# Performance work log

Measured on AMD Instinct MI355X. Metric: run time of the kernel, lower is better.

## Reference

```python
import jax, jax.numpy as jnp
import numpy as np

T_STEPS = 128
N_RAYS = 16384
RAY_EXT = 10.0  # ray_ext_factor


def _posenc(x, n_freq=4):
    # x: (...,3) in [-1,1] -> (...,3 + 3*2*n_freq) = (...,27)
    feats = [x]
    for k in range(n_freq):
        f = (2.0 ** k) * jnp.pi
        feats.append(jnp.sin(f * x))
        feats.append(jnp.cos(f * x))
    return jnp.concatenate(feats, -1)


def _sh_deg2(d):
    # real spherical harmonics, degree 0 and 1 (4 coeffs), d unit vectors (...,3)
    x, y, z = d[..., 0], d[..., 1], d[..., 2]
    c0 = 0.28209479177387814
    c1 = 0.4886025119029199
    return jnp.stack([jnp.full_like(x, c0), c1 * y, c1 * z, c1 * x], -1)


def _forward(rays_o, rays_d, tnoise, aabb, W1, b1, W2, b2, Wc1, bc1, Wc2, bc2):
    # --- ray-AABB intersection (slab method), RayBundle.intersect_aabb ---
    inv_d = 1.0 / rays_d
    t0 = (aabb[0] - rays_o) * inv_d
    t1 = (aabb[1] - rays_o) * inv_d
    tnear = jnp.maximum(jnp.max(jnp.minimum(t0, t1), -1, keepdims=True), 0.0)  # (N,1)
    tfar = jnp.min(jnp.maximum(t0, t1), -1, keepdims=True)                      # (N,1)
    active = (tfar > tnear).astype(rays_o.dtype)  # active_mask; masking replaces compaction

    # --- StratifiedRayStepSampler: ts (T,N,1) ---
    T = tnoise.shape[0]
    base = (jnp.arange(T, dtype=rays_o.dtype)[:, None, None] + tnoise) / T
    ts = tnear[None] + (tfar - tnear)[None] * base
    xyz = rays_o[None] + ts * rays_d[None]  # (T,N,3)

    # --- vol.sample(xyz, ynm, return_color=True): density + color MLP ---
    xn = 2.0 * (xyz - aabb[0]) / (aabb[1] - aabb[0]) - 1.0
    enc = _posenc(xn)                             # (T,N,27)
    h = jax.nn.relu(enc @ W1 + b1)                # (T,N,64)
    dh = h @ W2 + b2                              # (T,N,16)
    sigma = jnp.exp(dh[..., :1])                  # (T,N,1) density
    feat = dh[..., 1:]                            # (T,N,15)
    dnorm = jnp.linalg.norm(rays_d, axis=-1, keepdims=True)  # (N,1)
    ynm = _sh_deg2(rays_d / dnorm)                # encode_raydir -> (N,4)
    ynm = jnp.broadcast_to(ynm[None], (T,) + ynm.shape)      # expand to (T,N,4)
    hc = jax.nn.relu(jnp.concatenate([feat, ynm], -1) @ Wc1 + bc1)
    rgb = jax.nn.sigmoid(hc @ Wc2 + bc2)          # (T,N,3)

    # --- integrate_timesteps: transmittance-weighted compositing ---
    tfinal = tfar * RAY_EXT
    delta = jnp.concatenate([ts[1:] - ts[:-1], tfinal[None] - ts[-1:]], 0)  # (T,N,1)
    sd = sigma * delta * dnorm[None]
    alpha = 1.0 - jnp.exp(-sd)
    trans = jnp.exp(-(jnp.cumsum(sd, 0) - sd))    # exclusive cumsum transmittance
    w = trans * alpha * active[None]              # (T,N,1); inactive rays -> zero maps

    color = jnp.sum(w * rgb, 0)                   # color_map  (N,3)
    alpha_map = jnp.sum(w, 0)                     # alpha_map  (N,1)
    return jnp.concatenate([color, alpha_map], -1)  # rgba (N,4)


def setup_inputs() -> dict:
    key = jax.random.key(0)
    ks = jax.random.split(key, 8)
    # origins on a sphere of radius 2.5 around the unit aabb, aimed at points inside it
    o = jax.random.normal(ks[0], (N_RAYS, 3), jnp.float32)
    o = 2.5 * o / jnp.linalg.norm(o, axis=-1, keepdims=True)
    tgt = jax.random.uniform(ks[1], (N_RAYS, 3), jnp.float32, -0.5, 0.5)
    d = tgt - o
    d = d / jnp.linalg.norm(d, axis=-1, keepdims=True)
    aabb = jnp.array([[-1.0, -1.0, -1.0], [1.0, 1.0, 1.0]], jnp.float32)
    tnoise = jax.random.uniform(ks[2], (T_STEPS, N_RAYS, 1), jnp.float32)
    s1, s2, s3, s4 = 27 ** -0.5, 64 ** -0.5, 19 ** -0.5, 64 ** -0.5
    return {
        'rays_o': o, 'rays_d': d, 'tnoise': tnoise, 'aabb': aabb,
        'W1': jax.random.normal(ks[3], (27, 64), jnp.float32) * s1,
        'b1': jnp.zeros((64,), jnp.float32),
        'W2': jax.random.normal(ks[4], (64, 16), jnp.float32) * (0.1 * s2),
        'b2': jnp.zeros((16,), jnp.float32),
        'Wc1': jax.random.normal(ks[5], (19, 64), jnp.float32) * s3,
        'bc1': jnp.zeros((64,), jnp.float32),
        'Wc2': jax.random.normal(ks[6], (64, 3), jnp.float32) * s4,
        'bc2': jnp.zeros((3,), jnp.float32),
    }


def reference(rays_o, rays_d, tnoise, aabb, W1, b1, W2, b2, Wc1, bc1, Wc2, bc2):
    return _forward(rays_o, rays_d, tnoise, aabb, W1, b1, W2, b2, Wc1, bc1, Wc2, bc2)
```

## Files before the change

### kernel.cpp

```cpp
#include <hip/hip_runtime.h>
#include <stdint.h>

#define N_RAYS  16384
#define T_STEPS 128
#define RPW   16
#define WAVES 4
#define TSEG  32

typedef _Float16 half8  __attribute__((ext_vector_type(8)));
typedef _Float16 half4  __attribute__((ext_vector_type(4)));
typedef __fp16   fp16x2 __attribute__((ext_vector_type(2)));
typedef float    float4_ __attribute__((ext_vector_type(4)));
typedef uint32_t uint2_  __attribute__((ext_vector_type(2)));

#define H8_W1    0
#define H8_W2    256
#define H8_WC2   384
#define H_WC1K16 4096
#define F32_CV   3072
#define F32_BC2  3392
#define F32_S0   3408

__device__ __forceinline__ uint32_t pk(float a, float b) {
    fp16x2 h = __builtin_amdgcn_cvt_pkrtz(a, b);
    return __builtin_bit_cast(uint32_t, h);
}
__device__ __forceinline__ uint32_t pkr(float a, float b) {
    fp16x2 h = __builtin_amdgcn_cvt_pkrtz(a, b);
    fp16x2 z = {(__fp16)0.f, (__fp16)0.f};
    fp16x2 m = __builtin_elementwise_max(h, z);
    return __builtin_bit_cast(uint32_t, m);
}

__global__ void prep_weights(const float* __restrict__ W1, const float* __restrict__ b1,
                             const float* __restrict__ W2, const float* __restrict__ b2,
                             const float* __restrict__ Wc1, const float* __restrict__ bc1,
                             const float* __restrict__ Wc2, const float* __restrict__ bc2,
                             void* __restrict__ ws) {
    _Float16* wh = (_Float16*)ws;
    float*    wf = (float*)ws;
    int frag = blockIdx.x;
    int lane = threadIdx.x;
    int mm = lane & 15, q = lane >> 4;
    if (frag < 4) {
        int tau = frag;
        int n = tau * 16 + mm;
        for (int j = 0; j < 8; ++j) {
            float w;
            if (j < 6)      w = W1[(3 + 6 * q + j) * 64 + n];
            else if (j == 6) w = (q == 0) ? W1[0 * 64 + n] : (q == 1) ? W1[2 * 64 + n] : 0.f;
            else             w = (q == 0) ? W1[1 * 64 + n] : (q == 1) ? b1[n] : 0.f;
            wh[(H8_W1 + tau * 64 + lane) * 8 + j] = (_Float16)w;
        }
    } else if (frag < 6) {
        int kap = frag - 4;
        for (int j = 0; j < 8; ++j) {
            int k = kap * 32 + q * 8 + j;
            wh[(H8_W2 + kap * 64 + lane) * 8 + j] = (_Float16)W2[k * 16 + mm];
        }
    } else if (frag < 10) {
        int tau = frag - 6;
        int n2 = tau * 16 + mm;
        for (int j = 0; j < 4; ++j) {
            int k = 4 * q + j;
            float w = (k == 0) ? 0.f : Wc1[(k - 1) * 64 + n2];
            wh[H_WC1K16 + (tau * 64 + lane) * 4 + j] = (_Float16)w;
        }
    } else if (frag < 12) {
        int kap = frag - 10;
        for (int j = 0; j < 8; ++j) {
            int k = kap * 32 + q * 8 + j;
            wh[(H8_WC2 + kap * 64 + lane) * 8 + j] =
                (_Float16)((mm < 3) ? Wc2[k * 3 + mm] : 0.f);
        }
    } else {
        int n = lane;
        wf[F32_CV + 0 * 64 + n] = Wc1[15 * 64 + n];
        wf[F32_CV + 1 * 64 + n] = Wc1[16 * 64 + n];
        wf[F32_CV + 2 * 64 + n] = Wc1[17 * 64 + n];
        wf[F32_CV + 3 * 64 + n] = Wc1[18 * 64 + n];
        float cc = bc1[n];
        for (int c = 0; c < 15; ++c) cc += b2[1 + c] * Wc1[c * 64 + n];
        wf[F32_CV + 4 * 64 + n] = cc;
        if (lane < 16) wf[F32_BC2 + lane] = (lane < 3) ? bc2[lane] : 0.f;
        if (lane == 0) wf[F32_S0] = b2[0];
    }
}

__global__ __launch_bounds__(256, 4)
void render_kernel(const float* __restrict__ rays_o, const float* __restrict__ rays_d,
                   const float* __restrict__ tnoise, const float* __restrict__ aabb,
                   const void* __restrict__ ws, float* __restrict__ out) {
    __shared__ __align__(16) _Float16 sH[WAVES][2][1024];
    __shared__ float sComb[WAVES][RPW][5];

    const int tid  = threadIdx.x;
    const int wv   = tid >> 6;
    const int lane = tid & 63;
    const int m    = lane & 15;
    const int q    = lane >> 4;
    const int r    = blockIdx.x * RPW + m;

    const half8* wsv  = (const half8*)ws;
    const half4* wsv4 = (const half4*)((const _Float16*)ws + H_WC1K16);
    const float* wsf  = (const float*)ws;
    half8 fW1[4], fW2[2], fWc2[2];
    half4 fWc1[4];
    #pragma unroll
    for (int i = 0; i < 4; ++i) fW1[i]  = wsv[H8_W1  + i * 64 + lane];
    #pragma unroll
    for (int i = 0; i < 2; ++i) fW2[i]  = wsv[H8_W2  + i * 64 + lane];
    #pragma unroll
    for (int i = 0; i < 2; ++i) fWc2[i] = wsv[H8_WC2 + i * 64 + lane];
    #pragma unroll
    for (int i = 0; i < 4; ++i) fWc1[i] = wsv4[i * 64 + lane];
    const float4_ binit = ((const float4_*)(wsf + F32_BC2))[q];
    const float s0b = wsf[F32_S0];

    float o0 = rays_o[r * 3 + 0], o1 = rays_o[r * 3 + 1], o2 = rays_o[r * 3 + 2];
    float d0 = rays_d[r * 3 + 0], d1 = rays_d[r * 3 + 1], d2 = rays_d[r * 3 + 2];
    float a00 = aabb[0], a01 = aabb[1], a02 = aabb[2];
    float a10 = aabb[3], a11 = aabb[4], a12 = aabb[5];

    float i0 = 1.0f / d0, i1 = 1.0f / d1, i2 = 1.0f / d2;
    float u0 = (a00 - o0) * i0, v0 = (a10 - o0) * i0;
    float u1 = (a01 - o1) * i1, v1 = (a11 - o1) * i1;
    float u2 = (a02 - o2) * i2, v2 = (a12 - o2) * i2;
    float tnear = fmaxf(fmaxf(fmaxf(fminf(u0, v0), fminf(u1, v1)), fminf(u2, v2)), 0.0f);
    float tfar  = fminf(fminf(fmaxf(u0, v0), fmaxf(u1, v1)), fmaxf(u2, v2));
    bool active = (tfar > tnear);
    float dt = tfar - tnear;
    float dt128 = dt * (1.0f / 128.0f);

    float dn  = sqrtf(d0 * d0 + d1 * d1 + d2 * d2);
    float idn = 1.0f / dn;
    const float c0sh = 0.28209479177387814f;
    const float c1sh = 0.4886025119029199f;
    float y1 = c1sh * d1 * idn, y2 = c1sh * d2 * idn, y3 = c1sh * d0 * idn;

    float4_ cv[4];
    #pragma unroll
    for (int tau = 0; tau < 4; ++tau) {
        #pragma unroll
        for (int reg = 0; reg < 4; ++reg) {
            int n = tau * 16 + 4 * q + reg;
            float c = wsf[F32_CV + 4 * 64 + n];
            c = fmaf(c0sh, wsf[F32_CV + 0 * 64 + n], c);
            c = fmaf(y1,   wsf[F32_CV + 1 * 64 + n], c);
            c = fmaf(y2,   wsf[F32_CV + 2 * 64 + n], c);
            c = fmaf(y3,   wsf[F32_CV + 3 * 64 + n], c);
            cv[tau][reg] = c;
        }
    }

    float qs = 0.5f * (float)(1 << q);
    float sc0 = 2.0f / (a10 - a00), of0 = -a00 * sc0 - 1.0f;
    float sc1 = 2.0f / (a11 - a01), of1 = -a01 * sc1 - 1.0f;
    float sc2 = 2.0f / (a12 - a02), of2 = -a02 * sc2 - 1.0f;
    float scq0 = sc0 * qs, ofq0 = of0 * qs;
    float scq1 = sc1 * qs, ofq1 = of1 * qs;
    float scq2 = sc2 * qs, ofq2 = of2 * qs;

    _Float16*       hwp[2];
    const _Float16* hrp[2];
    #pragma unroll
    for (int p = 0; p < 2; ++p) {
        hwp[p] = &sH[wv][p][((q >> 1) * 16 + m) * 8 + 4 * (q & 1)];
        hrp[p] = &sH[wv][p][(q * 16 + m) * 8];
    }

    const float4_ z4 = {0.f, 0.f, 0.f, 0.f};
    const bool q0 = (q == 0), q1 = (q == 1);

    float trans = 1.0f, sdtot = 0.0f, wacc = 0.0f;
    float cacc0 = 0.0f, cacc1 = 0.0f, cacc2 = 0.0f;

    const int tbase = wv * TSEG;
    float nA = tnoise[(tbase + 0) * N_RAYS + r];
    float nB = tnoise[(tbase + 1) * N_RAYS + r];

    #pragma unroll 1
    for (int tt = 0; tt < TSEG; tt += 2) {
        const int t0 = tbase + tt, t1 = t0 + 1;
        float nC = (t0 + 2 < T_STEPS) ? tnoise[(t0 + 2) * N_RAYS + r] : 0.0f;
        float nD = (t0 + 3 < T_STEPS) ? tnoise[(t0 + 3) * N_RAYS + r] : 0.0f;
        float ts0 = fmaf((float)t0 + nA, dt128, tnear);
        float ts1 = fmaf((float)t1 + nB, dt128, tnear);
        float ts2 = fmaf((float)(t0 + 2) + nC, dt128, tnear);
        float tsP[2] = {ts0, ts1};
        float deltaP[2];
        deltaP[0] = ts1 - ts0;
        deltaP[1] = (t1 < T_STEPS - 1) ? (ts2 - ts1) : fmaf(tfar, 10.0f, -ts1);
        nA = nC; nB = nD;

        float dhx[2];
        float4_ rgbP[2];

        #pragma unroll
        for (int p = 0; p < 2; ++p) {
            float x = fmaf(tsP[p], d0, o0);
            float y = fmaf(tsP[p], d1, o1);
            float z = fmaf(tsP[p], d2, o2);
            float xr0 = fmaf(x, scq0, ofq0);
            float xr1 = fmaf(y, scq1, ofq1);
            float xr2 = fmaf(z, scq2, ofq2);
            float s0 = __builtin_amdgcn_sinf(xr0);
            float s1 = __builtin_amdgcn_sinf(xr1);
            float s2 = __builtin_amdgcn_sinf(xr2);
            float cA = __builtin_amdgcn_cosf(xr0);
            float cB = __builtin_amdgcn_cosf(xr1);
            float cC = __builtin_amdgcn_cosf(xr2);
            float e6 = q0 ? (xr0 + xr0) : (q1 ? xr2 : 0.0f);
            float e7 = q0 ? (xr1 + xr1) : (q1 ? 1.0f : 0.0f);
            union { uint32_t u[4]; half8 h; } xf_;
            xf_.u[0] = pk(s0, s1); xf_.u[1] = pk(s2, cA);
            xf_.u[2] = pk(cB, cC); xf_.u[3] = pk(e6, e7);
            half8 xf = xf_.h;

            float4_ h0 = __builtin_amdgcn_mfma_f32_16x16x32_f16(fW1[0], xf, z4, 0, 0, 0);
            float4_ h1 = __builtin_amdgcn_mfma_f32_16x16x32_f16(fW1[1], xf, z4, 0, 0, 0);
            float4_ h2 = __builtin_amdgcn_mfma_f32_16x16x32_f16(fW1[2], xf, z4, 0, 0, 0);
            float4_ h3 = __builtin_amdgcn_mfma_f32_16x16x32_f16(fW1[3], xf, z4, 0, 0, 0);
            uint2_ w;
            w.x = pkr(h0.x, h0.y); w.y = pkr(h0.z, h0.w); *(uint2_*)(hwp[p] + 0 * 256) = w;
            w.x = pkr(h1.x, h1.y); w.y = pkr(h1.z, h1.w); *(uint2_*)(hwp[p] + 1 * 256) = w;
            w.x = pkr(h2.x, h2.y); w.y = pkr(h2.z, h2.w); *(uint2_*)(hwp[p] + 2 * 256) = w;
            w.x = pkr(h3.x, h3.y); w.y = pkr(h3.z, h3.w); *(uint2_*)(hwp[p] + 3 * 256) = w;
        }

        #pragma unroll
        for (int p = 0; p < 2; ++p) {
            half8 hb0 = *(const half8*)(hrp[p] + 0);
            half8 hb1 = *(const half8*)(hrp[p] + 512);
            float4_ dh = __builtin_amdgcn_mfma_f32_16x16x32_f16(fW2[0], hb0, z4, 0, 0, 0);
            dh = __builtin_amdgcn_mfma_f32_16x16x32_f16(fW2[1], hb1, dh, 0, 0, 0);
            dhx[p] = dh.x;

            union { uint32_t u[2]; half4 h; } bf_;
            bf_.u[0] = pk(dh.x, dh.y); bf_.u[1] = pk(dh.z, dh.w);
            half4 fb = bf_.h;

            float4_ t0v = __builtin_amdgcn_mfma_f32_16x16x16f16(fWc1[0], fb, cv[0], 0, 0, 0);
            float4_ t1v = __builtin_amdgcn_mfma_f32_16x16x16f16(fWc1[1], fb, cv[1], 0, 0, 0);
            float4_ t2v = __builtin_amdgcn_mfma_f32_16x16x16f16(fWc1[2], fb, cv[2], 0, 0, 0);
            float4_ t3v = __builtin_amdgcn_mfma_f32_16x16x16f16(fWc1[3], fb, cv[3], 0, 0, 0);
            uint2_ w;
            w.x = pkr(t0v.x, t0v.y); w.y = pkr(t0v.z, t0v.w); *(uint2_*)(hwp[p] + 0 * 256) = w;
            w.x = pkr(t1v.x, t1v.y); w.y = pkr(t1v.z, t1v.w); *(uint2_*)(hwp[p] + 1 * 256) = w;
            w.x = pkr(t2v.x, t2v.y); w.y = pkr(t2v.z, t2v.w); *(uint2_*)(hwp[p] + 2 * 256) = w;
            w.x = pkr(t3v.x, t3v.y); w.y = pkr(t3v.z, t3v.w); *(uint2_*)(hwp[p] + 3 * 256) = w;
        }

        #pragma unroll
        for (int p = 0; p < 2; ++p) {
            half8 cb0 = *(const half8*)(hrp[p] + 0);
            half8 cb1 = *(const half8*)(hrp[p] + 512);
            float4_ rgbp = __builtin_amdgcn_mfma_f32_16x16x32_f16(fWc2[0], cb0, binit, 0, 0, 0);
            rgbP[p] = __builtin_amdgcn_mfma_f32_16x16x32_f16(fWc2[1], cb1, rgbp, 0, 0, 0);
        }

        if (q == 0) {
            #pragma unroll
            for (int p = 0; p < 2; ++p) {
                float sigma = __expf(dhx[p] + s0b);
                float sd = sigma * deltaP[p] * dn;
                float e = __expf(-sd);
                float alpha = 1.0f - e;
                float w = trans * alpha;
                float rr = __builtin_amdgcn_rcpf(1.0f + __expf(-rgbP[p].x));
                float rg = __builtin_amdgcn_rcpf(1.0f + __expf(-rgbP[p].y));
                float rb = __builtin_amdgcn_rcpf(1.0f + __expf(-rgbP[p].z));
                cacc0 = fmaf(w, rr, cacc0);
                cacc1 = fmaf(w, rg, cacc1);
                cacc2 = fmaf(w, rb, cacc2);
                wacc += w;
                trans *= e;
                sdtot += sd;
            }
        }
    }

    if (q == 0) {
        sComb[wv][m][0] = sdtot;
        sComb[wv][m][1] = wacc;
        sComb[wv][m][2] = cacc0;
        sComb[wv][m][3] = cacc1;
        sComb[wv][m][4] = cacc2;
    }
    __syncthreads();

    if (tid < RPW) {
        float P = 1.0f, C0 = 0.0f, C1 = 0.0f, C2 = 0.0f, WS = 0.0f;
        #pragma unroll
        for (int s = 0; s < WAVES; ++s) {
            C0 = fmaf(P, sComb[s][tid][2], C0);
            C1 = fmaf(P, sComb[s][tid][3], C1);
            C2 = fmaf(P, sComb[s][tid][4], C2);
            WS = fmaf(P, sComb[s][tid][1], WS);
            P *= __expf(-sComb[s][tid][0]);
        }
        float act = active ? 1.0f : 0.0f;
        const int rg = blockIdx.x * RPW + tid;
        out[rg * 4 + 0] = C0 * act;
        out[rg * 4 + 1] = C1 * act;
        out[rg * 4 + 2] = C2 * act;
        out[rg * 4 + 3] = WS * act;
    }
}

extern "C" void kernel_launch(void* const* d_in, const int* in_sizes, int n_in,
                              void* d_out, int out_size, void* d_ws, size_t ws_size,
                              hipStream_t stream) {
    const float* rays_o = (const float*)d_in[0];
    const float* rays_d = (const float*)d_in[1];
    const float* tnoise = (const float*)d_in[2];
    const float* aabb   = (const float*)d_in[3];
    const float* W1  = (const float*)d_in[4];
    const float* b1  = (const float*)d_in[5];
    const float* W2  = (const float*)d_in[6];
    const float* b2  = (const float*)d_in[7];
    const float* Wc1 = (const float*)d_in[8];
    const float* bc1 = (const float*)d_in[9];
    const float* Wc2 = (const float*)d_in[10];
    const float* bc2 = (const float*)d_in[11];

    prep_weights<<<dim3(13), dim3(64), 0, stream>>>(W1, b1, W2, b2, Wc1, bc1, Wc2, bc2, d_ws);

    dim3 grid(N_RAYS / RPW);
    dim3 block(WAVES * 64);
    render_kernel<<<grid, block, 0, stream>>>(rays_o, rays_d, tnoise, aabb, d_ws,
                                              (float*)d_out);
}
```

Measured before the change: 120.8 us.

## Chain MLP layers in registers via 16x16x16 MFMA, removing LDS round-trips

Instead of writing each layer's fp16 activations to shared memory and reading them back in the transposed B-operand layout for the next 16x16x32 MFMA, the weights for W2 and Wc2 are re-laid out in K=16 fragments. The MFMA output registers can then be packed directly into the next layer's B operand. This removes the LDS stores, loads and the shared buffer, at the cost of twice as many smaller MFMAs for W2 and Wc2 plus an extra vector add to combine the split accumulators.

```diff
diff --git a/kernel.cpp b/kernel.cpp
--- a/kernel.cpp
+++ b/kernel.cpp
@@ -11,11 +11,10 @@
 typedef _Float16 half4  __attribute__((ext_vector_type(4)));
 typedef __fp16   fp16x2 __attribute__((ext_vector_type(2)));
 typedef float    float4_ __attribute__((ext_vector_type(4)));
-typedef uint32_t uint2_  __attribute__((ext_vector_type(2)));
 
 #define H8_W1    0
-#define H8_W2    256
-#define H8_WC2   384
+#define H_W2K16  2048
+#define H_WC2K16 3072
 #define H_WC1K16 4096
 #define F32_CV   3072
 #define F32_BC2  3392
@@ -52,25 +51,25 @@
             else             w = (q == 0) ? W1[1 * 64 + n] : (q == 1) ? b1[n] : 0.f;
             wh[(H8_W1 + tau * 64 + lane) * 8 + j] = (_Float16)w;
         }
-    } else if (frag < 6) {
-        int kap = frag - 4;
-        for (int j = 0; j < 8; ++j) {
-            int k = kap * 32 + q * 8 + j;
-            wh[(H8_W2 + kap * 64 + lane) * 8 + j] = (_Float16)W2[k * 16 + mm];
-        }
-    } else if (frag < 10) {
-        int tau = frag - 6;
+    } else if (frag < 8) {
+        int tau = frag - 4;
+        for (int j = 0; j < 4; ++j) {
+            int k = tau * 16 + 4 * q + j;
+            wh[H_W2K16 + (tau * 64 + lane) * 4 + j] = (_Float16)W2[k * 16 + mm];
+        }
+    } else if (frag < 12) {
+        int tau = frag - 8;
         int n2 = tau * 16 + mm;
         for (int j = 0; j < 4; ++j) {
             int k = 4 * q + j;
             float w = (k == 0) ? 0.f : Wc1[(k - 1) * 64 + n2];
             wh[H_WC1K16 + (tau * 64 + lane) * 4 + j] = (_Float16)w;
         }
-    } else if (frag < 12) {
-        int kap = frag - 10;
-        for (int j = 0; j < 8; ++j) {
-            int k = kap * 32 + q * 8 + j;
-            wh[(H8_WC2 + kap * 64 + lane) * 8 + j] =
+    } else if (frag < 16) {
+        int tau = frag - 12;
+        for (int j = 0; j < 4; ++j) {
+            int k = tau * 16 + 4 * q + j;
+            wh[H_WC2K16 + (tau * 64 + lane) * 4 + j] =
                 (_Float16)((mm < 3) ? Wc2[k * 3 + mm] : 0.f);
         }
     } else {
@@ -91,7 +90,6 @@
 void render_kernel(const float* __restrict__ rays_o, const float* __restrict__ rays_d,
                    const float* __restrict__ tnoise, const float* __restrict__ aabb,
                    const void* __restrict__ ws, float* __restrict__ out) {
-    __shared__ __align__(16) _Float16 sH[WAVES][2][1024];
     __shared__ float sComb[WAVES][RPW][5];
 
     const int tid  = threadIdx.x;
@@ -102,18 +100,20 @@
     const int r    = blockIdx.x * RPW + m;
 
     const half8* wsv  = (const half8*)ws;
-    const half4* wsv4 = (const half4*)((const _Float16*)ws + H_WC1K16);
+    const half4* w2v  = (const half4*)((const _Float16*)ws + H_W2K16);
+    const half4* wc2v = (const half4*)((const _Float16*)ws + H_WC2K16);
+    const half4* wc1v = (const half4*)((const _Float16*)ws + H_WC1K16);
     const float* wsf  = (const float*)ws;
-    half8 fW1[4], fW2[2], fWc2[2];
-    half4 fWc1[4];
-    #pragma unroll
-    for (int i = 0; i < 4; ++i) fW1[i]  = wsv[H8_W1  + i * 64 + lane];
-    #pragma unroll
-    for (int i = 0; i < 2; ++i) fW2[i]  = wsv[H8_W2  + i * 64 + lane];
-    #pragma unroll
-    for (int i = 0; i < 2; ++i) fWc2[i] = wsv[H8_WC2 + i * 64 + lane];
-    #pragma unroll
-    for (int i = 0; i < 4; ++i) fWc1[i] = wsv4[i * 64 + lane];
+    half8 fW1[4];
+    half4 fW2[4], fWc1[4], fWc2[4];
+    #pragma unroll
+    for (int i = 0; i < 4; ++i) fW1[i]  = wsv[H8_W1 + i * 64 + lane];
+    #pragma unroll
+    for (int i = 0; i < 4; ++i) fW2[i]  = w2v[i * 64 + lane];
+    #pragma unroll
+    for (int i = 0; i < 4; ++i) fWc1[i] = wc1v[i * 64 + lane];
+    #pragma unroll
+    for (int i = 0; i < 4; ++i) fWc2[i] = wc2v[i * 64 + lane];
     const float4_ binit = ((const float4_*)(wsf + F32_BC2))[q];
     const float s0b = wsf[F32_S0];
 
@@ -160,14 +160,6 @@
     float scq0 = sc0 * qs, ofq0 = of0 * qs;
     float scq1 = sc1 * qs, ofq1 = of1 * qs;
     float scq2 = sc2 * qs, ofq2 = of2 * qs;
-
-    _Float16*       hwp[2];
-    const _Float16* hrp[2];
-    #pragma unroll
-    for (int p = 0; p < 2; ++p) {
-        hwp[p] = &sH[wv][p][((q >> 1) * 16 + m) * 8 + 4 * (q & 1)];
-        hrp[p] = &sH[wv][p][(q * 16 + m) * 8];
-    }
 
     const float4_ z4 = {0.f, 0.f, 0.f, 0.f};
     const bool q0 = (q == 0), q1 = (q == 1);
@@ -221,42 +213,41 @@
             float4_ h1 = __builtin_amdgcn_mfma_f32_16x16x32_f16(fW1[1], xf, z4, 0, 0, 0);
             float4_ h2 = __builtin_amdgcn_mfma_f32_16x16x32_f16(fW1[2], xf, z4, 0, 0, 0);
             float4_ h3 = __builtin_amdgcn_mfma_f32_16x16x32_f16(fW1[3], xf, z4, 0, 0, 0);
-            uint2_ w;
-            w.x = pkr(h0.x, h0.y); w.y = pkr(h0.z, h0.w); *(uint2_*)(hwp[p] + 0 * 256) = w;
-            w.x = pkr(h1.x, h1.y); w.y = pkr(h1.z, h1.w); *(uint2_*)(hwp[p] + 1 * 256) = w;
-            w.x = pkr(h2.x, h2.y); w.y = pkr(h2.z, h2.w); *(uint2_*)(hwp[p] + 2 * 256) = w;
-            w.x = pkr(h3.x, h3.y); w.y = pkr(h3.z, h3.w); *(uint2_*)(hwp[p] + 3 * 256) = w;
-        }
-
-        #pragma unroll
-        for (int p = 0; p < 2; ++p) {
-            half8 hb0 = *(const half8*)(hrp[p] + 0);
-            half8 hb1 = *(const half8*)(hrp[p] + 512);
-            float4_ dh = __builtin_amdgcn_mfma_f32_16x16x32_f16(fW2[0], hb0, z4, 0, 0, 0);
-            dh = __builtin_amdgcn_mfma_f32_16x16x32_f16(fW2[1], hb1, dh, 0, 0, 0);
+
+            union { uint32_t u[2]; half4 h; } hb0_, hb1_, hb2_, hb3_;
+            hb0_.u[0] = pkr(h0.x, h0.y); hb0_.u[1] = pkr(h0.z, h0.w);
+            hb1_.u[0] = pkr(h1.x, h1.y); hb1_.u[1] = pkr(h1.z, h1.w);
+            hb2_.u[0] = pkr(h2.x, h2.y); hb2_.u[1] = pkr(h2.z, h2.w);
+            hb3_.u[0] = pkr(h3.x, h3.y); hb3_.u[1] = pkr(h3.z, h3.w);
+
+            float4_ dA = __builtin_amdgcn_mfma_f32_16x16x16f16(fW2[0], hb0_.h, z4, 0, 0, 0);
+            float4_ dB = __builtin_amdgcn_mfma_f32_16x16x16f16(fW2[2], hb2_.h, z4, 0, 0, 0);
+            dA = __builtin_amdgcn_mfma_f32_16x16x16f16(fW2[1], hb1_.h, dA, 0, 0, 0);
+            dB = __builtin_amdgcn_mfma_f32_16x16x16f16(fW2[3], hb3_.h, dB, 0, 0, 0);
+            float4_ dh = dA + dB;
             dhx[p] = dh.x;
 
-            union { uint32_t u[2]; half4 h; } bf_;
-            bf_.u[0] = pk(dh.x, dh.y); bf_.u[1] = pk(dh.z, dh.w);
-            half4 fb = bf_.h;
+            union { uint32_t u[2]; half4 h; } fb_;
+            bf_pack: ;
+            fb_.u[0] = pk(dh.x, dh.y); fb_.u[1] = pk(dh.z, dh.w);
+            half4 fb = fb_.h;
 
             float4_ t0v = __builtin_amdgcn_mfma_f32_16x16x16f16(fWc1[0], fb, cv[0], 0, 0, 0);
             float4_ t1v = __builtin_amdgcn_mfma_f32_16x16x16f16(fWc1[1], fb, cv[1], 0, 0, 0);
             float4_ t2v = __builtin_amdgcn_mfma_f32_16x16x16f16(fWc1[2], fb, cv[2], 0, 0, 0);
             float4_ t3v = __builtin_amdgcn_mfma_f32_16x16x16f16(fWc1[3], fb, cv[3], 0, 0, 0);
-            uint2_ w;
-            w.x = pkr(t0v.x, t0v.y); w.y = pkr(t0v.z, t0v.w); *(uint2_*)(hwp[p] + 0 * 256) = w;
-            w.x = pkr(t1v.x, t1v.y); w.y = pkr(t1v.z, t1v.w); *(uint2_*)(hwp[p] + 1 * 256) = w;
-            w.x = pkr(t2v.x, t2v.y); w.y = pkr(t2v.z, t2v.w); *(uint2_*)(hwp[p] + 2 * 256) = w;
-            w.x = pkr(t3v.x, t3v.y); w.y = pkr(t3v.z, t3v.w); *(uint2_*)(hwp[p] + 3 * 256) = w;
-        }
-
-        #pragma unroll
-        for (int p = 0; p < 2; ++p) {
-            half8 cb0 = *(const half8*)(hrp[p] + 0);
-            half8 cb1 = *(const half8*)(hrp[p] + 512);
-            float4_ rgbp = __builtin_amdgcn_mfma_f32_16x16x32_f16(fWc2[0], cb0, binit, 0, 0, 0);
-            rgbP[p] = __builtin_amdgcn_mfma_f32_16x16x32_f16(fWc2[1], cb1, rgbp, 0, 0, 0);
+
+            union { uint32_t u[2]; half4 h; } cb0_, cb1_, cb2_, cb3_;
+            cb0_.u[0] = pkr(t0v.x, t0v.y); cb0_.u[1] = pkr(t0v.z, t0v.w);
+            cb1_.u[0] = pkr(t1v.x, t1v.y); cb1_.u[1] = pkr(t1v.z, t1v.w);
+            cb2_.u[0] = pkr(t2v.x, t2v.y); cb2_.u[1] = pkr(t2v.z, t2v.w);
+            cb3_.u[0] = pkr(t3v.x, t3v.y); cb3_.u[1] = pkr(t3v.z, t3v.w);
+
+            float4_ rA = __builtin_amdgcn_mfma_f32_16x16x16f16(fWc2[0], cb0_.h, binit, 0, 0, 0);
+            float4_ rB = __builtin_amdgcn_mfma_f32_16x16x16f16(fWc2[2], cb2_.h, z4, 0, 0, 0);
+            rA = __builtin_amdgcn_mfma_f32_16x16x16f16(fWc2[1], cb1_.h, rA, 0, 0, 0);
+            rB = __builtin_amdgcn_mfma_f32_16x16x16f16(fWc2[3], cb3_.h, rB, 0, 0, 0);
+            rgbP[p] = rA + rB;
         }
 
         if (q == 0) {
@@ -324,10 +315,10 @@
     const float* Wc2 = (const float*)d_in[10];
     const float* bc2 = (const float*)d_in[11];
 
-    prep_weights<<<dim3(13), dim3(64), 0, stream>>>(W1, b1, W2, b2, Wc1, bc1, Wc2, bc2, d_ws);
+    prep_weights<<<dim3(17), dim3(64), 0, stream>>>(W1, b1, W2, b2, Wc1, bc1, Wc2, bc2, d_ws);
 
     dim3 grid(N_RAYS / RPW);
     dim3 block(WAVES * 64);
-    render_kernel<<<grid, block, 0, stream>>>(rays_o, rays_d, tnoise, aabb, d_ws,
+    render_kernel<<<grid, block, 0, stream>>>(rays_o, rays_d, tnoise, aabb, ws_size ? d_ws : d_ws,
                                               (float*)d_out);
 }
```

Measured after the change: 124.1 us. 2.7% more time.
